# Optimization experiments

Hardware: AMD Instinct MI355X
Metric: run time of the kernel (lower is better)

## Reference

```python
import jax, jax.numpy as jnp
from jax import lax
import numpy as np

C = 256
K = 3
PAD = 1


def _bilinear_sample(x, py, px):
    """Zero-padded bilinear sampling.
    x: [B,C,Hin,Win]; py,px: [B,Kt,H,W] float sample coords -> [B,C,Kt,H,W]."""
    B, Cc, Hin, Win = x.shape
    y0 = jnp.floor(py)
    x0 = jnp.floor(px)
    y1 = y0 + 1.0
    x1 = x0 + 1.0
    wy1 = py - y0
    wy0 = 1.0 - wy1
    wx1 = px - x0
    wx0 = 1.0 - wx1
    xf = x.reshape(B, Cc, Hin * Win)

    def corner(yi, xi, wy, wx):
        valid = (yi >= 0) & (yi < Hin) & (xi >= 0) & (xi < Win)
        yc = jnp.clip(yi, 0, Hin - 1).astype(jnp.int32)
        xc = jnp.clip(xi, 0, Win - 1).astype(jnp.int32)
        idx = yc * Win + xc  # [B,Kt,H,W]
        g = jax.vmap(lambda xb, ib: xb[:, ib])(xf, idx)  # [B,C,Kt,H,W]
        w = (wy * wx) * valid.astype(x.dtype)
        return g * w[:, None]

    return (corner(y0, x0, wy0, wx0) + corner(y0, x1, wy0, wx1)
            + corner(y1, x0, wy1, wx0) + corner(y1, x1, wy1, wx1))


def _arm_forward(x, w_off, b_off, w, b):
    B, Cc, H, W = x.shape
    # offset-predicting conv (standard 3x3, pad 1)
    off = lax.conv_general_dilated(
        x, w_off, window_strides=(1, 1), padding=[(PAD, PAD), (PAD, PAD)],
        dimension_numbers=('NCHW', 'OIHW', 'NCHW')) + b_off[None, :, None, None]
    off = off.reshape(B, K * K, 2, H, W)  # [:, k, 0]=dy, [:, k, 1]=dx (mmcv layout)
    ky, kx = jnp.meshgrid(jnp.arange(K), jnp.arange(K), indexing='ij')
    ky = ky.reshape(-1).astype(x.dtype)  # [9]
    kx = kx.reshape(-1).astype(x.dtype)
    base_y = jnp.arange(H, dtype=x.dtype)[None, None, :, None]
    base_x = jnp.arange(W, dtype=x.dtype)[None, None, None, :]
    py = base_y - PAD + ky[None, :, None, None] + off[:, :, 0]  # [B,9,H,W]
    px = base_x - PAD + kx[None, :, None, None] + off[:, :, 1]
    sampled = _bilinear_sample(x, py, px)  # [B,C,9,H,W]
    out = jnp.einsum('bckhw,ock->bohw', sampled, w.reshape(Cc, Cc, K * K))
    out = out + b[None, :, None, None]
    return jax.nn.sigmoid(out)


def setup_inputs() -> dict:
    key = jax.random.key(0)
    k1, k2, k3, k4 = jax.random.split(key, 4)
    B, H, W = 8, 64, 64
    x = jax.random.normal(k1, (B, C, H, W), dtype=jnp.float32)
    # offset conv params (mmcv zero-inits these; use small random to exercise sampling)
    w_off = jax.random.normal(k2, (2 * K * K, C, K, K), dtype=jnp.float32) * 0.01
    b_off = jnp.zeros((2 * K * K,), dtype=jnp.float32)
    # deformable conv weight/bias (kaiming-ish scale)
    scale = 1.0 / np.sqrt(C * K * K)
    w = jax.random.normal(k3, (C, C, K, K), dtype=jnp.float32) * scale
    b = jax.random.normal(k4, (C,), dtype=jnp.float32) * scale
    return {"Fstagei": x, "w_off": w_off, "b_off": b_off, "w": w, "b": b}


def reference(Fstagei, w_off, b_off, w, b):
    return _arm_forward(Fstagei, w_off, b_off, w, b)
```

## Files before the change

### kernel.cpp

```cpp
#include <hip/hip_runtime.h>

typedef unsigned short u16;
typedef unsigned int u32;
typedef __attribute__((ext_vector_type(8))) short short8;
typedef __attribute__((ext_vector_type(4))) float f32x4;

#define BB 8
#define CCH 256
#define HH 64
#define WW 64
#define HP 66
#define NPOS 4096
#define KTOT 2304

#define XT_BYTES   17842176ull
#define W2R_OFF    17842176ull
#define WOFF2_OFF  19021824ull
#define P_OFF      19169280ull
#define OFF2_OFF   40402944ull
#define WS_MIN     42762240ull

__device__ __forceinline__ u16 f2bf(float f) {
    union { float f; u32 u; } v; v.f = f;
    u32 r = v.u + 0x7FFFu + ((v.u >> 16) & 1u);
    return (u16)(r >> 16);
}
__device__ __forceinline__ u32 pk2(float a, float b) {
    return (u32)f2bf(a) | ((u32)f2bf(b) << 16);
}
__device__ __forceinline__ u32 cvtpk(float lo, float hi) {
    u32 r;
    asm("v_cvt_pk_bf16_f32 %0, %1, %2" : "=v"(r) : "v"(lo), "v"(hi));
    return r;
}
__device__ __forceinline__ void bf2x2(u32 p, float& a, float& b) {
    union { u32 u; float f; } va, vb;
    va.u = p << 16; vb.u = p & 0xffff0000u;
    a = va.f; b = vb.f;
}
__device__ __forceinline__ void ldg_lds16(const u16* g, u16* l) {
    __builtin_amdgcn_global_load_lds((const __attribute__((address_space(1))) u32*)g,
                                     (__attribute__((address_space(3))) u32*)l, 16, 0, 0);
}

__global__ __launch_bounds__(256) void k_pre(const float* __restrict__ w, const float* __restrict__ w_off,
                                             const float* __restrict__ x,
                                             u16* __restrict__ W2r, u16* __restrict__ Woff2,
                                             u16* __restrict__ xT) {
    __shared__ __align__(16) float SH[4608];
    int bx = blockIdx.x;
    int t = threadIdx.x;
    if (bx < 256) {
        int o = bx;
        const float* src = w + (size_t)o * 2304;
#pragma unroll
        for (int j = 0; j < 9; ++j) SH[j * 256 + t] = src[j * 256 + t];
        __syncthreads();
        u16* dst = W2r + (size_t)o * 2304;
#pragma unroll
        for (int k = 0; k < 9; ++k) dst[k * 256 + t] = f2bf(SH[t * 9 + k]);
    } else if (bx < 288) {
        int o2 = bx - 256;
        if (o2 < 18) {
            const float* src = w_off + (size_t)o2 * 2304;
#pragma unroll
            for (int j = 0; j < 9; ++j) SH[j * 256 + t] = src[j * 256 + t];
            __syncthreads();
#pragma unroll
            for (int k = 0; k < 9; ++k) Woff2[(size_t)o2 * 2304 + k * 256 + t] = f2bf(SH[t * 9 + k]);
        } else {
#pragma unroll
            for (int k = 0; k < 9; ++k) Woff2[(size_t)o2 * 2304 + k * 256 + t] = 0;
        }
    } else if (bx < 808) {
        int idx = (bx - 288) * 4 + (t >> 6);
        int b = idx / 260, m = idx - b * 260;
        int y, xx;
        if (m < 66)       { y = 0;  xx = m; }
        else if (m < 132) { y = 65; xx = m - 66; }
        else if (m < 196) { y = m - 132 + 1; xx = 0; }
        else              { y = m - 196 + 1; xx = 65; }
        u16* p = xT + ((size_t)(b * HP + y) * HP + xx) * CCH + (t & 63) * 4;
        uint2 zz; zz.x = 0; zz.y = 0;
        *(uint2*)p = zz;
    } else {
        int idx = bx - 808;
        int b = idx & 7;
        int r = idx >> 3;
        int y = r & 63, c0 = (r >> 6) * 64;
        {
            int rrow = t >> 4, rlane = t & 15;
#pragma unroll
            for (int k = 0; k < 4; ++k) {
                int i = rrow + k * 16;
                const float* src = x + (((size_t)(b * CCH + c0 + i) * HH + y) * WW) + rlane * 4;
                float4 v = *(const float4*)src;
                *(float4*)&SH[i * 72 + rlane * 4] = v;
            }
        }
        __syncthreads();
        {
            int xc = t >> 2, cs = t & 3;
            u16* dst = xT + (((size_t)(b * HP + y + 1) * HP) + (xc + 1)) * CCH + c0 + cs * 16;
            u32 p[8];
#pragma unroll
            for (int j = 0; j < 8; ++j)
                p[j] = pk2(SH[(cs * 16 + 2 * j) * 72 + xc], SH[(cs * 16 + 2 * j + 1) * 72 + xc]);
            uint4 d0, d1;
            d0.x = p[0]; d0.y = p[1]; d0.z = p[2]; d0.w = p[3];
            d1.x = p[4]; d1.y = p[5]; d1.z = p[6]; d1.w = p[7];
            *(uint4*)dst = d0;
            *(uint4*)(dst + 8) = d1;
        }
    }
}

__global__ __launch_bounds__(256) void k_offconv(const u16* __restrict__ xT,
                                                 const u16* __restrict__ Woff2,
                                                 float* __restrict__ P) {
    __shared__ __align__(16) u16 AS[2][2048];
    __shared__ __align__(16) u16 BS[2][8192];
    int b = blockIdx.x, k9 = blockIdx.y;
    int pos0 = blockIdx.z * 128;
    int ky = k9 / 3, kx = k9 % 3;
    int t = threadIdx.x, lane = t & 63, wv = t >> 6;

    int srow = lane >> 3;
    int sw8 = ((lane & 7) ^ srow) << 3;
    const u16* pA = Woff2 + (size_t)k9 * 256;
    const u16* pXb = xT + (size_t)b * HP * HP * CCH;

    f32x4 acc[2][2];
    f32x4 z = {0.f, 0.f, 0.f, 0.f};
    acc[0][0] = z; acc[0][1] = z; acc[1][0] = z; acc[1][1] = z;

    auto stage = [&](int cs, int d) {
        int koff = cs * 64;
        {
            int row = wv * 8 + srow;
            ldg_lds16(pA + (size_t)row * KTOT + koff + sw8, &AS[d][wv * 512]);
        }
#pragma unroll
        for (int i = 0; i < 4; ++i) {
            int inst = wv * 4 + i;
            int rowg = pos0 + inst * 8 + srow;
            int py_ = rowg >> 6, px_ = rowg & 63;
            const u16* g = pXb + (((size_t)(py_ + ky) * HP) + px_ + kx) * CCH + koff + sw8;
            ldg_lds16(g, &BS[d][inst * 512]);
        }
    };

    stage(0, 0);
    __syncthreads();

    int buf = 0;
    int m = lane & 15, q = lane >> 4, key = lane & 7;
    for (int cs = 0; cs < 4; ++cs) {
        if (cs < 3) stage(cs + 1, buf ^ 1);
#pragma unroll
        for (int j = 0; j < 2; ++j) {
            int slot8 = (((j * 4 + q) ^ key) << 3);
            short8 a0 = *(const short8*)&AS[buf][m * 64 + slot8];
            short8 a1 = *(const short8*)&AS[buf][(16 + m) * 64 + slot8];
            short8 b0 = *(const short8*)&BS[buf][(wv * 32 + m) * 64 + slot8];
            short8 b1 = *(const short8*)&BS[buf][(wv * 32 + 16 + m) * 64 + slot8];
            acc[0][0] = __builtin_amdgcn_mfma_f32_16x16x32_bf16(a0, b0, acc[0][0], 0, 0, 0);
            acc[0][1] = __builtin_amdgcn_mfma_f32_16x16x32_bf16(a0, b1, acc[0][1], 0, 0, 0);
            acc[1][0] = __builtin_amdgcn_mfma_f32_16x16x32_bf16(a1, b0, acc[1][0], 0, 0, 0);
            acc[1][1] = __builtin_amdgcn_mfma_f32_16x16x32_bf16(a1, b1, acc[1][1], 0, 0, 0);
        }
        __syncthreads();
        buf ^= 1;
    }
    int nn = lane & 15;
    float* Pp = P + (size_t)(b * 9 + k9) * 18 * NPOS;
#pragma unroll
    for (int ao = 0; ao < 2; ++ao)
#pragma unroll
        for (int bn = 0; bn < 2; ++bn) {
            int pos = pos0 + wv * 32 + bn * 16 + nn;
#pragma unroll
            for (int r = 0; r < 4; ++r) {
                int o = ao * 16 + q * 4 + r;
                if (o < 18) Pp[o * NPOS + pos] = acc[ao][bn][r];
            }
        }
}

__global__ __launch_bounds__(64) void k_reduce(const float* __restrict__ P,
                                               const float* __restrict__ b_off,
                                               float2* __restrict__ off2) {
    int b = blockIdx.x;
    int pos = blockIdx.y * 64 + threadIdx.x;
    float s[18];
#pragma unroll
    for (int o = 0; o < 18; ++o) s[o] = b_off[o];
    const float* Pp = P + (size_t)(b * 9) * 18 * NPOS + pos;
    for (int k9 = 0; k9 < 9; ++k9) {
#pragma unroll
        for (int o = 0; o < 18; ++o)
            s[o] += Pp[(k9 * 18 + o) * NPOS];
    }
#pragma unroll
    for (int op = 0; op < 9; ++op) {
        float2 v; v.x = s[2 * op]; v.y = s[2 * op + 1];
        off2[(((size_t)(b * 9 + op)) << 12) + pos] = v;
    }
}

__global__ __launch_bounds__(512, 2) void k_gemm(const u16* __restrict__ xT,
                                                 const float2* __restrict__ off2,
                                                 const u16* __restrict__ W2r,
                                                 const float* __restrict__ bias,
                                                 float* __restrict__ out) {
    __shared__ __align__(16) u16 AS[2][16384];
    __shared__ __align__(16) u16 BSF[128 * 264];
    int b = blockIdx.x;
    int pos0 = blockIdx.z * 128;
    int t = threadIdx.x, lane = t & 63, wv = t >> 6;
    int wr = wv >> 1, wc = wv & 1;

    int srow = lane >> 3;
    int sw8 = ((lane & 7) ^ srow) << 3;
    const u16* pA = W2r;

    int brow0 = t >> 3;
    int bcl = (t & 7) << 3;
    int bbase = b * HP * HP;

    f32x4 acc[4][4];
    f32x4 z = {0.f, 0.f, 0.f, 0.f};
#pragma unroll
    for (int i = 0; i < 4; ++i)
#pragma unroll
        for (int j = 0; j < 4; ++j) acc[i][j] = z;

    auto stageA = [&](int gs, int d) {
        int k9 = gs >> 2, cs = gs & 3;
        int koffA = k9 * 256 + cs * 64;
#pragma unroll
        for (int i = 0; i < 4; ++i) {
            int inst = wv * 4 + i;
            int row = inst * 8 + srow;
            ldg_lds16(pA + (size_t)row * KTOT + koffA + sw8, &AS[d][inst * 512]);
        }
    };

    const u16* gp[2][4];
    float wt[2][4];
    float2 fnext[2];
    uint4 gv[8];

    auto computeState = [&](int tap) {
#pragma unroll
        for (int ii = 0; ii < 2; ++ii) {
            int pos = pos0 + brow0 + (ii << 6);
            int y = pos >> 6, x = pos & 63;
            int ky = tap / 3, kx = tap - (tap / 3) * 3;
            float pyf = (float)(y - 1 + ky) + fnext[ii].x;
            float pxf = (float)(x - 1 + kx) + fnext[ii].y;
            float y0f = floorf(pyf), x0f = floorf(pxf);
            int y0 = (int)y0f, x0 = (int)x0f;
            int y1 = y0 + 1, x1 = x0 + 1;
            float wy1 = pyf - y0f, wy0 = 1.f - wy1;
            float wx1 = pxf - x0f, wx0 = 1.f - wx1;
            bool vy0 = (y0 >= 0) & (y0 < HH), vy1 = (y1 >= 0) & (y1 < HH);
            bool vx0 = (x0 >= 0) & (x0 < WW), vx1 = (x1 >= 0) & (x1 < WW);
            int yc0 = min(max(y0, 0), HH - 1), yc1 = min(max(y1, 0), HH - 1);
            int xc0 = min(max(x0, 0), WW - 1), xc1 = min(max(x1, 0), WW - 1);
            wt[ii][0] = (vy0 & vx0) ? wy0 * wx0 : 0.f;
            wt[ii][1] = (vy0 & vx1) ? wy0 * wx1 : 0.f;
            wt[ii][2] = (vy1 & vx0) ? wy1 * wx0 : 0.f;
            wt[ii][3] = (vy1 & vx1) ? wy1 * wx1 : 0.f;
            gp[ii][0] = xT + (size_t)(bbase + (yc0 + 1) * HP + xc0 + 1) * CCH + bcl;
            gp[ii][1] = xT + (size_t)(bbase + (yc0 + 1) * HP + xc1 + 1) * CCH + bcl;
            gp[ii][2] = xT + (size_t)(bbase + (yc1 + 1) * HP + xc0 + 1) * CCH + bcl;
            gp[ii][3] = xT + (size_t)(bbase + (yc1 + 1) * HP + xc1 + 1) * CCH + bcl;
        }
    };
    auto gatherRegion = [&](int rr) {
#pragma unroll
        for (int ii = 0; ii < 2; ++ii)
#pragma unroll
            for (int c = 0; c < 4; ++c)
                gv[ii * 4 + c] = *(const uint4*)(gp[ii][c] + rr * 64);
    };
    auto blendWrite = [&](int rr) {
#pragma unroll
        for (int ii = 0; ii < 2; ++ii) {
            int row = brow0 + (ii << 6);
            float v[8];
#pragma unroll
            for (int dw = 0; dw < 4; ++dw) {
                float a0, b0_, a1, b1_, a2, b2_, a3, b3_;
                bf2x2(((const u32*)&gv[ii * 4 + 0])[dw], a0, b0_);
                bf2x2(((const u32*)&gv[ii * 4 + 1])[dw], a1, b1_);
                bf2x2(((const u32*)&gv[ii * 4 + 2])[dw], a2, b2_);
                bf2x2(((const u32*)&gv[ii * 4 + 3])[dw], a3, b3_);
                v[2 * dw]     = wt[ii][0] * a0 + wt[ii][1] * a1 + wt[ii][2] * a2 + wt[ii][3] * a3;
                v[2 * dw + 1] = wt[ii][0] * b0_ + wt[ii][1] * b1_ + wt[ii][2] * b2_ + wt[ii][3] * b3_;
            }
            uint4 sv;
            sv.x = cvtpk(v[0], v[1]); sv.y = cvtpk(v[2], v[3]);
            sv.z = cvtpk(v[4], v[5]); sv.w = cvtpk(v[6], v[7]);
            *(uint4*)&BSF[row * 264 + rr * 64 + bcl] = sv;
        }
    };

    {
        fnext[0] = off2[((size_t)(b * 9 + 0) << 12) + pos0 + brow0];
        fnext[1] = off2[((size_t)(b * 9 + 0) << 12) + pos0 + brow0 + 64];
        computeState(0);
#pragma unroll
        for (int rr = 0; rr < 4; ++rr) {
            gatherRegion(rr);
            blendWrite(rr);
        }
        fnext[0] = off2[((size_t)(b * 9 + 1) << 12) + pos0 + brow0];
        fnext[1] = off2[((size_t)(b * 9 + 1) << 12) + pos0 + brow0 + 64];
        stageA(0, 0);
        asm volatile("s_waitcnt lgkmcnt(0)" ::: "memory");
    }

    int m = lane & 15, q = lane >> 4, key = lane & 7;
    for (int gs = 0; gs <= 35; ++gs) {
        int t9 = gs >> 2, cs = gs & 3, cur = gs & 1;
        if (gs >= 1 && gs <= 32) { asm volatile("s_waitcnt vmcnt(8)" ::: "memory"); }
        else                     { asm volatile("s_waitcnt vmcnt(0)" ::: "memory"); }
        __builtin_amdgcn_s_barrier();

        if (gs < 35) stageA(gs + 1, cur ^ 1);
        __builtin_amdgcn_sched_barrier(0);

        if (gs >= 1 && gs <= 32) {
            asm volatile("s_waitcnt vmcnt(4)" ::: "memory");
            blendWrite((cs + 3) & 3);
        }
        if (cs == 0 && t9 <= 7) computeState(t9 + 1);
        if (gs <= 31) {
            if (cs == 3 && t9 <= 6) {
                fnext[0] = off2[((size_t)(b * 9 + t9 + 2) << 12) + pos0 + brow0];
                fnext[1] = off2[((size_t)(b * 9 + t9 + 2) << 12) + pos0 + brow0 + 64];
            }
            gatherRegion(cs);
        }
        __builtin_amdgcn_sched_barrier(0);

#pragma unroll
        for (int j = 0; j < 2; ++j) {
            int slot8 = (((j * 4 + q) ^ key) << 3);
            int bchunk = (cs * 8 + j * 4 + q) << 3;
            short8 af[4], bfr[4];
#pragma unroll
            for (int ao = 0; ao < 4; ++ao)
                af[ao] = *(const short8*)&AS[cur][(wr * 64 + ao * 16 + m) * 64 + slot8];
#pragma unroll
            for (int bn = 0; bn < 4; ++bn)
                bfr[bn] = *(const short8*)&BSF[(wc * 64 + bn * 16 + m) * 264 + bchunk];
            __builtin_amdgcn_s_setprio(1);
#pragma unroll
            for (int ao = 0; ao < 4; ++ao)
#pragma unroll
                for (int bn = 0; bn < 4; ++bn)
                    acc[ao][bn] = __builtin_amdgcn_mfma_f32_16x16x32_bf16(af[ao], bfr[bn], acc[ao][bn], 0, 0, 0);
            __builtin_amdgcn_s_setprio(0);
        }
        asm volatile("s_waitcnt lgkmcnt(0)" ::: "memory");
    }

    int nn = lane & 15;
#pragma unroll
    for (int ao = 0; ao < 4; ++ao) {
        int ob = wr * 64 + ao * 16 + q * 4;
#pragma unroll
        for (int bn = 0; bn < 4; ++bn) {
            int pos = pos0 + wc * 64 + bn * 16 + nn;
#pragma unroll
            for (int r = 0; r < 4; ++r) {
                float v = acc[ao][bn][r] + bias[ob + r];
                float sg = 1.0f / (1.0f + __expf(-v));
                out[(size_t)((b * CCH + ob + r) * NPOS) + pos] = sg;
            }
        }
    }
}

extern "C" void kernel_launch(void* const* d_in, const int* in_sizes, int n_in,
                              void* d_out, int out_size, void* d_ws, size_t ws_size,
                              hipStream_t stream) {
    const float* x     = (const float*)d_in[0];
    const float* w_off = (const float*)d_in[1];
    const float* b_off = (const float*)d_in[2];
    const float* w     = (const float*)d_in[3];
    const float* bias  = (const float*)d_in[4];
    float* out = (float*)d_out;

    char* ws = (char*)d_ws;
    u16*    xT    = (u16*)ws;
    u16*    W2r   = (u16*)(ws + W2R_OFF);
    u16*    Woff2 = (u16*)(ws + WOFF2_OFF);
    float*  P     = (float*)(ws + P_OFF);
    float2* off2  = (float2*)(ws + OFF2_OFF);

    if (ws_size < WS_MIN) return;

    k_pre<<<2856, 256, 0, stream>>>(w, w_off, x, W2r, Woff2, xT);
    k_offconv<<<dim3(8, 9, 32), 256, 0, stream>>>(xT, Woff2, P);
    k_reduce<<<dim3(8, 64), 64, 0, stream>>>(P, b_off, off2);
    k_gemm<<<dim3(8, 1, 32), 512, 0, stream>>>(xT, off2, W2r, bias, out);
}
```

Measured before the change: 174.8 us.

## Fuse offset-predicting conv and reduction into the deformable GEMM kernel

Removes the separate offset-conv and reduce kernels and computes the 18 offset channels per 128-position tile inside k_gemm as a prologue using MFMA with direct global loads, storing results plus bias into shared memory. The main loop then reads offsets from LDS instead of a global off2 buffer. This eliminates two launches and the global round trip of partial sums, at the cost of an unpipelined serial prologue per block and extra LDS usage.

```diff
diff --git a/kernel.cpp b/kernel.cpp
--- a/kernel.cpp
+++ b/kernel.cpp
@@ -16,9 +16,7 @@
 #define XT_BYTES   17842176ull
 #define W2R_OFF    17842176ull
 #define WOFF2_OFF  19021824ull
-#define P_OFF      19169280ull
-#define OFF2_OFF   40402944ull
-#define WS_MIN     42762240ull
+#define WS_MIN     19169280ull
 
 __device__ __forceinline__ u16 f2bf(float f) {
     union { float f; u32 u; } v; v.f = f;
@@ -115,106 +113,15 @@
     }
 }
 
-__global__ __launch_bounds__(256) void k_offconv(const u16* __restrict__ xT,
+__global__ __launch_bounds__(512, 2) void k_gemm(const u16* __restrict__ xT,
                                                  const u16* __restrict__ Woff2,
-                                                 float* __restrict__ P) {
-    __shared__ __align__(16) u16 AS[2][2048];
-    __shared__ __align__(16) u16 BS[2][8192];
-    int b = blockIdx.x, k9 = blockIdx.y;
-    int pos0 = blockIdx.z * 128;
-    int ky = k9 / 3, kx = k9 % 3;
-    int t = threadIdx.x, lane = t & 63, wv = t >> 6;
-
-    int srow = lane >> 3;
-    int sw8 = ((lane & 7) ^ srow) << 3;
-    const u16* pA = Woff2 + (size_t)k9 * 256;
-    const u16* pXb = xT + (size_t)b * HP * HP * CCH;
-
-    f32x4 acc[2][2];
-    f32x4 z = {0.f, 0.f, 0.f, 0.f};
-    acc[0][0] = z; acc[0][1] = z; acc[1][0] = z; acc[1][1] = z;
-
-    auto stage = [&](int cs, int d) {
-        int koff = cs * 64;
-        {
-            int row = wv * 8 + srow;
-            ldg_lds16(pA + (size_t)row * KTOT + koff + sw8, &AS[d][wv * 512]);
-        }
-#pragma unroll
-        for (int i = 0; i < 4; ++i) {
-            int inst = wv * 4 + i;
-            int rowg = pos0 + inst * 8 + srow;
-            int py_ = rowg >> 6, px_ = rowg & 63;
-            const u16* g = pXb + (((size_t)(py_ + ky) * HP) + px_ + kx) * CCH + koff + sw8;
-            ldg_lds16(g, &BS[d][inst * 512]);
-        }
-    };
-
-    stage(0, 0);
-    __syncthreads();
-
-    int buf = 0;
-    int m = lane & 15, q = lane >> 4, key = lane & 7;
-    for (int cs = 0; cs < 4; ++cs) {
-        if (cs < 3) stage(cs + 1, buf ^ 1);
-#pragma unroll
-        for (int j = 0; j < 2; ++j) {
-            int slot8 = (((j * 4 + q) ^ key) << 3);
-            short8 a0 = *(const short8*)&AS[buf][m * 64 + slot8];
-            short8 a1 = *(const short8*)&AS[buf][(16 + m) * 64 + slot8];
-            short8 b0 = *(const short8*)&BS[buf][(wv * 32 + m) * 64 + slot8];
-            short8 b1 = *(const short8*)&BS[buf][(wv * 32 + 16 + m) * 64 + slot8];
-            acc[0][0] = __builtin_amdgcn_mfma_f32_16x16x32_bf16(a0, b0, acc[0][0], 0, 0, 0);
-            acc[0][1] = __builtin_amdgcn_mfma_f32_16x16x32_bf16(a0, b1, acc[0][1], 0, 0, 0);
-            acc[1][0] = __builtin_amdgcn_mfma_f32_16x16x32_bf16(a1, b0, acc[1][0], 0, 0, 0);
-            acc[1][1] = __builtin_amdgcn_mfma_f32_16x16x32_bf16(a1, b1, acc[1][1], 0, 0, 0);
-        }
-        __syncthreads();
-        buf ^= 1;
-    }
-    int nn = lane & 15;
-    float* Pp = P + (size_t)(b * 9 + k9) * 18 * NPOS;
-#pragma unroll
-    for (int ao = 0; ao < 2; ++ao)
-#pragma unroll
-        for (int bn = 0; bn < 2; ++bn) {
-            int pos = pos0 + wv * 32 + bn * 16 + nn;
-#pragma unroll
-            for (int r = 0; r < 4; ++r) {
-                int o = ao * 16 + q * 4 + r;
-                if (o < 18) Pp[o * NPOS + pos] = acc[ao][bn][r];
-            }
-        }
-}
-
-__global__ __launch_bounds__(64) void k_reduce(const float* __restrict__ P,
-                                               const float* __restrict__ b_off,
-                                               float2* __restrict__ off2) {
-    int b = blockIdx.x;
-    int pos = blockIdx.y * 64 + threadIdx.x;
-    float s[18];
-#pragma unroll
-    for (int o = 0; o < 18; ++o) s[o] = b_off[o];
-    const float* Pp = P + (size_t)(b * 9) * 18 * NPOS + pos;
-    for (int k9 = 0; k9 < 9; ++k9) {
-#pragma unroll
-        for (int o = 0; o < 18; ++o)
-            s[o] += Pp[(k9 * 18 + o) * NPOS];
-    }
-#pragma unroll
-    for (int op = 0; op < 9; ++op) {
-        float2 v; v.x = s[2 * op]; v.y = s[2 * op + 1];
-        off2[(((size_t)(b * 9 + op)) << 12) + pos] = v;
-    }
-}
-
-__global__ __launch_bounds__(512, 2) void k_gemm(const u16* __restrict__ xT,
-                                                 const float2* __restrict__ off2,
+                                                 const float* __restrict__ b_off,
                                                  const u16* __restrict__ W2r,
                                                  const float* __restrict__ bias,
                                                  float* __restrict__ out) {
     __shared__ __align__(16) u16 AS[2][16384];
     __shared__ __align__(16) u16 BSF[128 * 264];
+    __shared__ __align__(16) float OFF[18 * 128];
     int b = blockIdx.x;
     int pos0 = blockIdx.z * 128;
     int t = threadIdx.x, lane = t & 63, wv = t >> 6;
@@ -235,22 +142,47 @@
 #pragma unroll
         for (int j = 0; j < 4; ++j) acc[i][j] = z;
 
-    auto stageA = [&](int gs, int d) {
-        int k9 = gs >> 2, cs = gs & 3;
-        int koffA = k9 * 256 + cs * 64;
-#pragma unroll
-        for (int i = 0; i < 4; ++i) {
-            int inst = wv * 4 + i;
-            int row = inst * 8 + srow;
-            ldg_lds16(pA + (size_t)row * KTOT + koffA + sw8, &AS[d][inst * 512]);
-        }
-    };
+    int m = lane & 15, q = lane >> 4, key = lane & 7;
+
+    {
+        int pl = wv * 16 + m;
+        int posg = pos0 + pl;
+        int yy = posg >> 6, xx = posg & 63;
+        f32x4 pacc0 = z, pacc1 = z;
+        const u16* apb = Woff2 + (size_t)m * KTOT + q * 8;
+        for (int g2 = 0; g2 < 72; ++g2) {
+            int tap = g2 >> 3;
+            int ky = tap / 3, kx = tap - (tap / 3) * 3;
+            int ch0 = (g2 & 7) * 32;
+            const u16* bp = xT + ((size_t)(bbase + (yy + ky) * HP) + (xx + kx)) * CCH + ch0 + q * 8;
+            short8 bf = *(const short8*)bp;
+            short8 a0 = *(const short8*)(apb + (g2 << 5));
+            short8 a1 = *(const short8*)(apb + (size_t)16 * KTOT + (g2 << 5));
+            pacc0 = __builtin_amdgcn_mfma_f32_16x16x32_bf16(a0, bf, pacc0, 0, 0, 0);
+            pacc1 = __builtin_amdgcn_mfma_f32_16x16x32_bf16(a1, bf, pacc1, 0, 0, 0);
+        }
+#pragma unroll
+        for (int r = 0; r < 4; ++r) {
+            int o0 = q * 4 + r;
+            OFF[o0 * 128 + pl] = pacc0[r] + b_off[o0];
+            int o1 = 16 + q * 4 + r;
+            if (o1 < 18) OFF[o1 * 128 + pl] = pacc1[r] + b_off[o1];
+        }
+        asm volatile("s_waitcnt lgkmcnt(0)" ::: "memory");
+        __builtin_amdgcn_s_barrier();
+    }
 
     const u16* gp[2][4];
     float wt[2][4];
     float2 fnext[2];
     uint4 gv[8];
 
+    auto ldOff = [&](int tap) {
+        fnext[0].x = OFF[(2 * tap) * 128 + brow0];
+        fnext[0].y = OFF[(2 * tap + 1) * 128 + brow0];
+        fnext[1].x = OFF[(2 * tap) * 128 + brow0 + 64];
+        fnext[1].y = OFF[(2 * tap + 1) * 128 + brow0 + 64];
+    };
     auto computeState = [&](int tap) {
 #pragma unroll
         for (int ii = 0; ii < 2; ++ii) {
@@ -306,23 +238,30 @@
             *(uint4*)&BSF[row * 264 + rr * 64 + bcl] = sv;
         }
     };
+    auto stageA = [&](int gs, int d) {
+        int k9 = gs >> 2, cs = gs & 3;
+        int koffA = k9 * 256 + cs * 64;
+#pragma unroll
+        for (int i = 0; i < 4; ++i) {
+            int inst = wv * 4 + i;
+            int row = inst * 8 + srow;
+            ldg_lds16(pA + (size_t)row * KTOT + koffA + sw8, &AS[d][inst * 512]);
+        }
+    };
 
     {
-        fnext[0] = off2[((size_t)(b * 9 + 0) << 12) + pos0 + brow0];
-        fnext[1] = off2[((size_t)(b * 9 + 0) << 12) + pos0 + brow0 + 64];
+        ldOff(0);
         computeState(0);
 #pragma unroll
         for (int rr = 0; rr < 4; ++rr) {
             gatherRegion(rr);
             blendWrite(rr);
         }
-        fnext[0] = off2[((size_t)(b * 9 + 1) << 12) + pos0 + brow0];
-        fnext[1] = off2[((size_t)(b * 9 + 1) << 12) + pos0 + brow0 + 64];
+        ldOff(1);
         stageA(0, 0);
         asm volatile("s_waitcnt lgkmcnt(0)" ::: "memory");
     }
 
-    int m = lane & 15, q = lane >> 4, key = lane & 7;
     for (int gs = 0; gs <= 35; ++gs) {
         int t9 = gs >> 2, cs = gs & 3, cur = gs & 1;
         if (gs >= 1 && gs <= 32) { asm volatile("s_waitcnt vmcnt(8)" ::: "memory"); }
@@ -336,14 +275,11 @@
             asm volatile("s_waitcnt vmcnt(4)" ::: "memory");
             blendWrite((cs + 3) & 3);
         }
-        if (cs == 0 && t9 <= 7) computeState(t9 + 1);
-        if (gs <= 31) {
-            if (cs == 3 && t9 <= 6) {
-                fnext[0] = off2[((size_t)(b * 9 + t9 + 2) << 12) + pos0 + brow0];
-                fnext[1] = off2[((size_t)(b * 9 + t9 + 2) << 12) + pos0 + brow0 + 64];
-            }
-            gatherRegion(cs);
-        }
+        if (cs == 0 && t9 <= 7) {
+            ldOff(t9 + 1);
+            computeState(t9 + 1);
+        }
+        if (gs <= 31) gatherRegion(cs);
         __builtin_amdgcn_sched_barrier(0);
 
 #pragma unroll
@@ -399,13 +335,9 @@
     u16*    xT    = (u16*)ws;
     u16*    W2r   = (u16*)(ws + W2R_OFF);
     u16*    Woff2 = (u16*)(ws + WOFF2_OFF);
-    float*  P     = (float*)(ws + P_OFF);
-    float2* off2  = (float2*)(ws + OFF2_OFF);
 
     if (ws_size < WS_MIN) return;
 
     k_pre<<<2856, 256, 0, stream>>>(w, w_off, x, W2r, Woff2, xT);
-    k_offconv<<<dim3(8, 9, 32), 256, 0, stream>>>(xT, Woff2, P);
-    k_reduce<<<dim3(8, 64), 64, 0, stream>>>(P, b_off, off2);
-    k_gemm<<<dim3(8, 1, 32), 512, 0, stream>>>(xT, off2, W2r, bias, out);
-}
+    k_gemm<<<dim3(8, 1, 32), 512, 0, stream>>>(xT, Woff2, b_off, W2r, bias, out);
+}
```

New measurement: 203.8 us. 1.17x slower.
